# Performance work log

Measured on AMD Instinct MI355X. Metric: run time of the kernel, lower is better.

## Reference

```python
import jax, jax.numpy as jnp
import numpy as np

F_, V, ED = 16, 1000, 16
B = 65536
D_IN = F_ * ED            # 256
STAR = [256, 512, 256]    # star layers
FCN = [256, 128, 64]      # mmoe expert layers
DOM, TSK, EXP = 3, 2, 8
KDT = DOM * TSK           # 6 gates/towers
SKIP_WEIGHT = 0.5
EPS = 1e-5


def layernorm(x, g, b):
    mu = jnp.mean(x, -1, keepdims=True)
    var = jnp.mean((x - mu) ** 2, -1, keepdims=True)
    return (x - mu) * jax.lax.rsqrt(var + EPS) * g + b


def mlp1(x, W, b, g, be):
    # Linear -> LayerNorm -> ReLU (MLP_N with one block)
    return jax.nn.relu(layernorm(x @ W + b, g, be))


def stack2(h, W1, b1, g1, be1, W2, b2, g2, be2):
    # vectorized bank of 2-block MLP_N experts; h: [B,D0], W1: [E,D0,D1]
    h1 = jax.nn.relu(layernorm(jnp.einsum('bd,edh->ebh', h, W1) + b1[:, None, :], g1[:, None, :], be1[:, None, :]))
    h2 = jax.nn.relu(layernorm(jnp.einsum('ebd,edh->ebh', h1, W2) + b2[:, None, :], g2[:, None, :], be2[:, None, :]))
    return h2  # [E,B,H]


def setup_inputs() -> dict:
    key = jax.random.key(0)
    ks = iter(jax.random.split(key, 64))

    def nrm(shape, scale=0.05):
        return jax.random.normal(next(ks), shape, jnp.float32) * scale

    inp = {}
    inp['x'] = jax.random.randint(next(ks), (F_, B), 0, 3).astype(jnp.int32)
    inp['emb_tables'] = nrm((F_, V, ED))
    inp['skip_W'] = nrm((D_IN, STAR[2])); inp['skip_b'] = jnp.zeros((STAR[2],))
    inp['skip_g'] = jnp.ones((STAR[2],)); inp['skip_be'] = jnp.zeros((STAR[2],))
    inp['shared_W'] = nrm((STAR[0], STAR[1])); inp['shared_b'] = jnp.zeros((STAR[1],))
    inp['slot_W'] = nrm((DOM, STAR[0], STAR[1])); inp['slot_b'] = jnp.zeros((DOM, STAR[1]))
    inp['star_W'] = nrm((STAR[1], STAR[2])); inp['star_b'] = jnp.zeros((STAR[2],))
    inp['star_g'] = jnp.ones((STAR[2],)); inp['star_be'] = jnp.zeros((STAR[2],))
    inp['dskip_W'] = nrm((KDT, STAR[2], FCN[-1])); inp['dskip_b'] = jnp.zeros((KDT, FCN[-1]))
    inp['dskip_g'] = jnp.ones((KDT, FCN[-1])); inp['dskip_be'] = jnp.zeros((KDT, FCN[-1]))
    for pre, n in (('exp', EXP), ('dexp', DOM), ('texp', TSK)):
        inp[pre + '_W1'] = nrm((n, FCN[0], FCN[1])); inp[pre + '_b1'] = jnp.zeros((n, FCN[1]))
        inp[pre + '_g1'] = jnp.ones((n, FCN[1])); inp[pre + '_be1'] = jnp.zeros((n, FCN[1]))
        inp[pre + '_W2'] = nrm((n, FCN[1], FCN[2])); inp[pre + '_b2'] = jnp.zeros((n, FCN[2]))
        inp[pre + '_g2'] = jnp.ones((n, FCN[2])); inp[pre + '_be2'] = jnp.zeros((n, FCN[2]))
    inp['gate_W'] = nrm((KDT, FCN[0], EXP)); inp['gate_b'] = jnp.zeros((KDT, EXP))
    inp['tow_W1'] = nrm((KDT, FCN[-1], FCN[-1])); inp['tow_b1'] = jnp.zeros((KDT, FCN[-1]))
    inp['tow_g'] = jnp.ones((KDT, FCN[-1])); inp['tow_be'] = jnp.zeros((KDT, FCN[-1]))
    inp['tow_W2'] = nrm((KDT, FCN[-1])); inp['tow_b2'] = jnp.zeros((KDT,))
    return inp


def _forward(x, emb_tables, skip_W, skip_b, skip_g, skip_be, shared_W, shared_b,
             slot_W, slot_b, star_W, star_b, star_g, star_be,
             dskip_W, dskip_b, dskip_g, dskip_be,
             exp_W1, exp_b1, exp_g1, exp_be1, exp_W2, exp_b2, exp_g2, exp_be2,
             dexp_W1, dexp_b1, dexp_g1, dexp_be1, dexp_W2, dexp_b2, dexp_g2, dexp_be2,
             texp_W1, texp_b1, texp_g1, texp_be1, texp_W2, texp_b2, texp_g2, texp_be2,
             gate_W, gate_b, tow_W1, tow_b1, tow_g, tow_be, tow_W2, tow_b2):
    domain_id = x[-1]                                          # [B] in {0,1,2}
    embs = jax.vmap(lambda t, i: t[i])(emb_tables, x)          # [F,B,ED]
    input_emb = jnp.moveaxis(embs, 0, 1).reshape(x.shape[1], D_IN)  # [B,256]

    skip = mlp1(input_emb, skip_W, skip_b, skip_g, skip_be)    # [B,256]

    # STAR: per-domain elementwise-product weights, domain masked select
    slot_out = jnp.einsum('bd,kdh->kbh', input_emb, slot_W * shared_W[None]) + slot_b[:, None, :] + shared_b  # [D,B,512]
    onehot = (domain_id[None, :] == jnp.arange(DOM)[:, None]).astype(slot_out.dtype)  # [D,B]
    emb0 = jnp.sum(onehot[:, :, None] * slot_out, axis=0)      # [B,512]
    emb = mlp1(emb0, star_W, star_b, star_g, star_be) + skip   # [B,256]

    # gates use emb.detach()
    gate = jax.nn.softmax(jnp.einsum('bd,kde->kbe', jax.lax.stop_gradient(emb), gate_W) + gate_b[:, None, :], axis=-1)  # [6,B,8]

    fea = stack2(emb, exp_W1, exp_b1, exp_g1, exp_be1, exp_W2, exp_b2, exp_g2, exp_be2)        # [8,B,64]
    dfea = stack2(emb, dexp_W1, dexp_b1, dexp_g1, dexp_be1, dexp_W2, dexp_b2, dexp_g2, dexp_be2)  # [3,B,64]
    tfea = stack2(emb, texp_W1, texp_b1, texp_g1, texp_be1, texp_W2, texp_b2, texp_g2, texp_be2)  # [2,B,64]
    dskip = jax.nn.relu(layernorm(jnp.einsum('bd,kdh->kbh', emb, dskip_W) + dskip_b[:, None, :], dskip_g[:, None, :], dskip_be[:, None, :]))  # [6,B,64]

    d_idx = jnp.arange(KDT) % DOM
    t_idx = jnp.arange(KDT) % TSK
    fused = jnp.einsum('kbe,ebh->kbh', gate, fea) + dfea[d_idx] + tfea[t_idx] + SKIP_WEIGHT * dskip  # [6,B,64]

    h = jax.nn.relu(layernorm(jnp.einsum('kbh,khj->kbj', fused, tow_W1) + tow_b1[:, None, :], tow_g[:, None, :], tow_be[:, None, :]))
    probs = jax.nn.sigmoid(jnp.einsum('kbh,kh->kb', h, tow_W2) + tow_b2[:, None])  # [6,B]

    # output[:, i] with i = t*DOM + d -> [B,T,D]; pick per-sample domain column
    out = jnp.moveaxis(probs, 0, 1).reshape(-1, TSK, DOM)
    result = jnp.take_along_axis(out, domain_id[:, None, None].astype(jnp.int32), axis=2)[:, :, 0]  # [B,T]
    return result


def reference(x, emb_tables, skip_W, skip_b, skip_g, skip_be, shared_W, shared_b,
              slot_W, slot_b, star_W, star_b, star_g, star_be,
              dskip_W, dskip_b, dskip_g, dskip_be,
              exp_W1, exp_b1, exp_g1, exp_be1, exp_W2, exp_b2, exp_g2, exp_be2,
              dexp_W1, dexp_b1, dexp_g1, dexp_be1, dexp_W2, dexp_b2, dexp_g2, dexp_be2,
              texp_W1, texp_b1, texp_g1, texp_be1, texp_W2, texp_b2, texp_g2, texp_be2,
              gate_W, gate_b, tow_W1, tow_b1, tow_g, tow_be, tow_W2, tow_b2):
    return _forward(x, emb_tables, skip_W, skip_b, skip_g, skip_be, shared_W, shared_b,
                    slot_W, slot_b, star_W, star_b, star_g, star_be,
                    dskip_W, dskip_b, dskip_g, dskip_be,
                    exp_W1, exp_b1, exp_g1, exp_be1, exp_W2, exp_b2, exp_g2, exp_be2,
                    dexp_W1, dexp_b1, dexp_g1, dexp_be1, dexp_W2, dexp_b2, dexp_g2, dexp_be2,
                    texp_W1, texp_b1, texp_g1, texp_be1, texp_W2, texp_b2, texp_g2, texp_be2,
                    gate_W, gate_b, tow_W1, tow_b1, tow_g, tow_be, tow_W2, tow_b2)
```

## Files before the change

kernel.cpp:

```cpp
#include <hip/hip_runtime.h>
#include <stdint.h>

#define B_TOT 65536

typedef __attribute__((ext_vector_type(8))) short s16x8;
typedef __attribute__((ext_vector_type(4))) float f32x4;
typedef unsigned short u16;
typedef unsigned int u32;
typedef unsigned long long u64;

#define OFF_SKIPW   0
#define OFF_MD      65536
#define OFF_GATEW   262144
#define OFF_EXPW1   274432
#define OFF_EXPW2   700416
#define OFF_DSKIPW  806912
#define OFF_TOWW1   905216
#define OFF_BVEC    929792
#define OFF_PAR     931328
#define OFF_PARF    941568
#define OFF_EMB     944640
#define OFF_PERM    17852928
#define OFF_CNT     17985024

#define PAR_DSK  7488
#define PAR_TOW  8640
#define PAR_GB   10176
#define PAR_TB2  10224

__device__ __forceinline__ float bf2f(u16 h){ u32 v=((u32)h)<<16; return __builtin_bit_cast(float,v); }
__device__ __forceinline__ u16 f2bf(float f){
  u32 u=__builtin_bit_cast(u32,f);
  u += 0x7fffu + ((u>>16)&1u);
  return (u16)(u>>16);
}
__device__ __forceinline__ f32x4 mfma16(s16x8 a, s16x8 b, f32x4 c){
  return __builtin_amdgcn_mfma_f32_16x16x32_bf16(a,b,c,0,0,0);
}
__device__ __forceinline__ void lds_fence(){ asm volatile("s_waitcnt lgkmcnt(0)" ::: "memory"); }

__device__ __forceinline__ void gstage(const u16* gsrc, u16* ldsdst, int nbytes, int wv, int lane, int nw){
  for(int off = wv*1024; off < nbytes; off += nw*1024){
    __builtin_amdgcn_global_load_lds(
      (const __attribute__((address_space(1))) u32*)((const char*)gsrc + off + lane*16),
      (__attribute__((address_space(3))) u32*)((char*)ldsdst + off),
      16, 0, 0);
  }
}

template<int NT>
__device__ __forceinline__ void ln16(const f32x4* a, float invN, float* mu, float* rs){
  float s[4], q[4];
#pragma unroll
  for(int r=0;r<4;r++){ float aa=0.f,bb=0.f;
#pragma unroll
    for(int t=0;t<NT;t++){ float v=a[t][r]; aa+=v; bb+=v*v; }
    s[r]=aa; q[r]=bb; }
#pragma unroll
  for(int m=1;m<16;m<<=1){
#pragma unroll
    for(int r=0;r<4;r++){ s[r]+=__shfl_xor(s[r],m,16); q[r]+=__shfl_xor(q[r],m,16); } }
#pragma unroll
  for(int r=0;r<4;r++){ float m_=s[r]*invN; float v=q[r]*invN-m_*m_; mu[r]=m_; rs[r]=rsqrtf(v+1e-5f); }
}

__global__ __launch_bounds__(64) void k_sortinit(u16* __restrict__ ws){
  if(threadIdx.x<8) ((u32*)(ws+OFF_CNT))[threadIdx.x]=0u;
}
__global__ __launch_bounds__(256) void k_count(const int* __restrict__ x, u16* __restrict__ ws){
  u32* cnt=(u32*)(ws+OFF_CNT);
  int i=blockIdx.x*256+threadIdx.x;
  int lane=threadIdx.x&63;
  int d=x[15*B_TOT+i];
  u64 m0=__ballot(d==0), m1=__ballot(d==1), m2=__ballot(d==2);
  if(lane==0){
    if(m0) atomicAdd(&cnt[0],(u32)__popcll(m0));
    if(m1) atomicAdd(&cnt[1],(u32)__popcll(m1));
    if(m2) atomicAdd(&cnt[2],(u32)__popcll(m2));
  }
}
__global__ __launch_bounds__(256) void k_scatter(const int* __restrict__ x, u16* __restrict__ ws){
  u32* cnt=(u32*)(ws+OFF_CNT);
  u32* perm=(u32*)(ws+OFF_PERM);
  int i=blockIdx.x*256+threadIdx.x;
  int lane=threadIdx.x&63;
  int d=x[15*B_TOT+i];
  u32 c0=cnt[0], c1=cnt[1];
  u32 s1=c0, s2=c0+c1;
  u64 m0=__ballot(d==0), m1=__ballot(d==1), m2=__ballot(d==2);
  u32 b0v=0,b1v=0,b2v=0;
  if(lane==0){
    if(m0) b0v=atomicAdd(&cnt[3],(u32)__popcll(m0));
    if(m1) b1v=atomicAdd(&cnt[4],(u32)__popcll(m1));
    if(m2) b2v=atomicAdd(&cnt[5],(u32)__popcll(m2));
  }
  b0v=__shfl(b0v,0,64); b1v=__shfl(b1v,0,64); b2v=__shfl(b2v,0,64);
  u64 below=(1ull<<lane)-1ull;
  u32 pos;
  if(d==0)      pos=    b0v+(u32)__popcll(m0&below);
  else if(d==1) pos=s1+ b1v+(u32)__popcll(m1&below);
  else          pos=s2+ b2v+(u32)__popcll(m2&below);
  perm[pos]=(u32)i;
}

__global__ __launch_bounds__(256) void k_pack(
    const float* __restrict__ skip_W, const float* __restrict__ gate_W,
    const float* __restrict__ exp_W1, const float* __restrict__ dexp_W1, const float* __restrict__ texp_W1,
    const float* __restrict__ exp_W2, const float* __restrict__ dexp_W2, const float* __restrict__ texp_W2,
    const float* __restrict__ dskip_W, const float* __restrict__ tow_W1,
    u16* __restrict__ ws)
{
  int i=blockIdx.x*256+threadIdx.x;
  if(i>=OFF_BVEC) return;
  if(i>=OFF_MD && i<OFF_GATEW) return;
  float v;
  if(i<OFF_MD){
    int l=i; int j=l&7, lane=(l>>3)&63, kt=(l>>9)&7, ct=l>>12;
    int n=ct*16+(lane&15), k=kt*32+((lane>>4)<<3)+j;
    v = skip_W[k*256+n];
  } else if(i<OFF_EXPW1){
    int l=i-OFF_GATEW; int j=l&7, lane=(l>>3)&63, kt=(l>>9)&7, ct=l>>12;
    int n=ct*16+(lane&15), k=kt*32+((lane>>4)<<3)+j;
    int k6=n>>3, e=n&7;
    v = gate_W[(k6*256+k)*8+e];
  } else if(i<OFF_EXPW2){
    int l=i-OFF_EXPW1; int e=l>>15, r=l&32767;
    int j=r&7, lane=(r>>3)&63, kt=(r>>9)&7, ct=r>>12;
    int n=ct*16+(lane&15), k=kt*32+((lane>>4)<<3)+j;
    v = (e<8)? exp_W1[(e*256+k)*128+n] : (e<11)? dexp_W1[((e-8)*256+k)*128+n] : texp_W1[((e-11)*256+k)*128+n];
  } else if(i<OFF_DSKIPW){
    int l=i-OFF_EXPW2; int e=l>>13, r=l&8191;
    int j=r&7, lane=(r>>3)&63, kt=(r>>9)&3, ct=r>>11;
    int n=ct*16+(lane&15), k=kt*32+((lane>>4)<<3)+j;
    v = (e<8)? exp_W2[(e*128+k)*64+n] : (e<11)? dexp_W2[((e-8)*128+k)*64+n] : texp_W2[((e-11)*128+k)*64+n];
  } else if(i<OFF_TOWW1){
    int l=i-OFF_DSKIPW; int s=l>>14, r=l&16383;
    int j=r&7, lane=(r>>3)&63, kt=(r>>9)&7, ct=r>>12;
    int n=ct*16+(lane&15), k=kt*32+((lane>>4)<<3)+j;
    v = dskip_W[(s*256+k)*64+n];
  } else {
    int l=i-OFF_TOWW1; int s=l>>12, r=l&4095;
    int j=r&7, lane=(r>>3)&63, kt=(r>>9)&1, ct=r>>10;
    int n=ct*16+(lane&15), k=kt*32+((lane>>4)<<3)+j;
    v = tow_W1[(s*64+k)*64+n];
  }
  ws[i]=f2bf(v);
}

__global__ __launch_bounds__(256) void k_packpar(
    const float* __restrict__ exp_b1,const float* __restrict__ exp_g1,const float* __restrict__ exp_be1,
    const float* __restrict__ exp_b2,const float* __restrict__ exp_g2,const float* __restrict__ exp_be2,
    const float* __restrict__ dexp_b1,const float* __restrict__ dexp_g1,const float* __restrict__ dexp_be1,
    const float* __restrict__ dexp_b2,const float* __restrict__ dexp_g2,const float* __restrict__ dexp_be2,
    const float* __restrict__ texp_b1,const float* __restrict__ texp_g1,const float* __restrict__ texp_be1,
    const float* __restrict__ texp_b2,const float* __restrict__ texp_g2,const float* __restrict__ texp_be2,
    const float* __restrict__ dskip_b,const float* __restrict__ dskip_g,const float* __restrict__ dskip_be,
    const float* __restrict__ gate_b,
    const float* __restrict__ tow_b1,const float* __restrict__ tow_g,const float* __restrict__ tow_be,
    const float* __restrict__ tow_W2,const float* __restrict__ tow_b2,
    const float* __restrict__ skip_b,const float* __restrict__ skip_g,const float* __restrict__ skip_be,
    const float* __restrict__ star_b,const float* __restrict__ star_g,const float* __restrict__ star_be,
    u16* __restrict__ ws)
{
  int i=blockIdx.x*256+threadIdx.x;
  float* parf=(float*)(ws+OFF_PARF);
  if(i<10240){
    float v=0.f;
    if(i<PAR_DSK){
      int e=i/576, r=i%576;
      const float *b1,*g1,*be1,*b2,*g2,*be2;
      if(e<8){ b1=exp_b1+e*128; g1=exp_g1+e*128; be1=exp_be1+e*128;
               b2=exp_b2+e*64;  g2=exp_g2+e*64;  be2=exp_be2+e*64; }
      else if(e<11){ int q=e-8; b1=dexp_b1+q*128; g1=dexp_g1+q*128; be1=dexp_be1+q*128;
               b2=dexp_b2+q*64; g2=dexp_g2+q*64; be2=dexp_be2+q*64; }
      else { int q=e-11; b1=texp_b1+q*128; g1=texp_g1+q*128; be1=texp_be1+q*128;
               b2=texp_b2+q*64; g2=texp_g2+q*64; be2=texp_be2+q*64; }
      v = (r<128)? b1[r] : (r<256)? g1[r-128] : (r<384)? be1[r-256]
        : (r<448)? b2[r-384] : (r<512)? g2[r-448] : be2[r-512];
    } else if(i<PAR_TOW){
      int l=i-PAR_DSK; int j=l/192, r=l%192;
      v = (r<64)? dskip_b[j*64+r] : (r<128)? dskip_g[j*64+r-64] : dskip_be[j*64+r-128];
    } else if(i<PAR_GB){
      int l=i-PAR_TOW; int k6=l/256, r=l%256;
      v = (r<64)? tow_b1[k6*64+r] : (r<128)? tow_g[k6*64+r-64]
        : (r<192)? tow_be[k6*64+r-128] : tow_W2[k6*64+r-192];
    } else if(i<PAR_TB2){ v=gate_b[i-PAR_GB]; }
    else if(i<PAR_TB2+6){ v=tow_b2[i-PAR_TB2]; }
    ws[OFF_PAR+i]=f2bf(v);
  } else if(i<10240+1536){
    int l=i-10240;
    parf[l] = (l<256)? skip_b[l] : (l<512)? skip_g[l-256] : (l<768)? skip_be[l-512]
            : (l<1024)? star_b[l-768] : (l<1280)? star_g[l-1024] : star_be[l-1280];
  }
}

__global__ __launch_bounds__(256) void k_fold(
    const float* __restrict__ slot_W, const float* __restrict__ shared_W, const float* __restrict__ star_W,
    const float* __restrict__ slot_b, const float* __restrict__ shared_b,
    u16* __restrict__ ws)
{
  __shared__ float w[512];
  int bid=blockIdx.x, tid=threadIdx.x;
  if(bid<768){
    int d=bid>>8, k=bid&255;
    for(int j=tid;j<512;j+=256) w[j]=slot_W[(d*256+k)*512+j]*shared_W[k*512+j];
    __syncthreads();
    int n=tid; float a=0.f;
    for(int j=0;j<512;j++) a += w[j]*star_W[j*256+n];
    int ct=n>>4, l15=n&15, kt=k>>5, hi=(k>>3)&3, j8=k&7;
    ws[OFF_MD + d*65536 + (((ct*8+kt)*64 + hi*16 + l15)<<3) + j8] = f2bf(a);
  } else {
    int d=bid-768;
    for(int j=tid;j<512;j+=256) w[j]=slot_b[d*512+j]+shared_b[j];
    __syncthreads();
    int n=tid; float a=0.f;
    for(int j=0;j<512;j++) a += w[j]*star_W[j*256+n];
    ((float*)(ws+OFF_BVEC))[d*256+n]=a;
  }
}

__global__ __launch_bounds__(256,2) void k_front(
    const int* __restrict__ x, const float* __restrict__ emb_tables,
    u16* __restrict__ wsu)
{
  __shared__ __align__(16) u16 shbuf[33792];
  __shared__ float bvecL[768];
  __shared__ float parF[1536];

  const int tid=threadIdx.x, lane=tid&63, wv=tid>>6;
  const int l15=lane&15, hq=lane>>4;
  const int b0=blockIdx.x*128, rowbase=b0+wv*32;
  const f32x4 fz={0.f,0.f,0.f,0.f};
  const s16x8 zf={0,0,0,0,0,0,0,0};
  u16* Wb[2]={shbuf, shbuf+8192};
  u16* trbw = shbuf + wv*8448;
  u16* embp = wsu+OFF_EMB;
  const u32* perm=(const u32*)(wsu+OFF_PERM);

  gstage(wsu+OFF_SKIPW, Wb[0], 16384, wv, lane, 4);
  gstage(wsu+OFF_BVEC, (u16*)bvecL, 3072, wv, lane, 4);
  gstage(wsu+OFF_PARF, (u16*)parF, 6144, wv, lane, 4);

  const int dlo=__builtin_amdgcn_readfirstlane(x[15*B_TOT+(int)perm[b0]]);
  const int dhi=__builtin_amdgcn_readfirstlane(x[15*B_TOT+(int)perm[b0+127]]);

  int dmA[2], dm[2][4];
  s16x8 af[2][8];
#pragma unroll
  for(int rt=0;rt<2;rt++){
    int prow=(int)perm[rowbase+rt*16+l15];
    dmA[rt]=x[15*B_TOT+prow];
#pragma unroll
    for(int r=0;r<4;r++) dm[rt][r]=x[15*B_TOT+(int)perm[rowbase+rt*16+hq*4+r]];
#pragma unroll
    for(int kt=0;kt<8;kt++){
      int f=kt*2+(hq>>1), j0=(hq&1)*8;
      int idx=x[f*B_TOT+prow];
      const float* sp=emb_tables + (size_t)(f*1000+idx)*16 + j0;
      float4 v0=*(const float4*)sp, v1=*(const float4*)(sp+4);
      union{ u16 h[8]; s16x8 v; } t;
      t.h[0]=f2bf(v0.x); t.h[1]=f2bf(v0.y); t.h[2]=f2bf(v0.z); t.h[3]=f2bf(v0.w);
      t.h[4]=f2bf(v1.x); t.h[5]=f2bf(v1.y); t.h[6]=f2bf(v1.z); t.h[7]=f2bf(v1.w);
      af[rt][kt]=t.v;
    }
  }
  __syncthreads();
  int cur=0;

  f32x4 acc[2][16];
#pragma unroll
  for(int rt=0;rt<2;rt++)
#pragma unroll
    for(int ct=0;ct<16;ct++) acc[rt][ct]=fz;

#pragma unroll
  for(int c=0;c<8;c++){
    if(c<7) gstage(wsu+OFF_SKIPW+(c+1)*8192, Wb[cur^1], 16384, wv, lane, 4);
    const u16* B=Wb[cur];
#pragma unroll
    for(int kt=0;kt<8;kt++){
#pragma unroll
      for(int i=0;i<2;i++){
        s16x8 bf=*(const s16x8*)(B + (((i*8+kt)*64+lane)<<3));
        acc[0][c*2+i]=mfma16(af[0][kt],bf,acc[0][c*2+i]);
        acc[1][c*2+i]=mfma16(af[1][kt],bf,acc[1][c*2+i]);
      }
    }
    __syncthreads(); cur^=1;
  }
#pragma unroll
  for(int rt=0;rt<2;rt++){
#pragma unroll
    for(int ct=0;ct<16;ct++){ float bb=parF[ct*16+l15];
#pragma unroll
      for(int r=0;r<4;r++) acc[rt][ct][r]+=bb; }
    float mu[4],rs[4];
    ln16<16>(&acc[rt][0], 1.f/256.f, mu, rs);
#pragma unroll
    for(int ct=0;ct<16;ct++){
      int col=ct*16+l15;
      float gv=parF[256+col], bev=parF[512+col];
#pragma unroll
      for(int r=0;r<4;r++){
        float v=fmaxf((acc[rt][ct][r]-mu[r])*rs[r]*gv+bev,0.f);
        trbw[(rt*16+hq*4+r)*264 + col]=f2bf(v);
      }
    }
  }
  lds_fence();
#pragma unroll
  for(int rt=0;rt<2;rt++){
    int rtg=(b0>>4)+wv*2+rt;
#pragma unroll
    for(int kt=0;kt<8;kt++){
      s16x8 v=*(const s16x8*)(trbw + (rt*16+l15)*264 + kt*32+hq*8);
      *(s16x8*)(embp + (((size_t)(rtg*8+kt)*64+lane)<<3)) = v;
    }
  }
  __syncthreads();
  gstage(wsu+OFF_MD+dlo*65536, Wb[0], 16384, wv, lane, 4);
  __syncthreads();
  cur=0;

#pragma unroll
  for(int rt=0;rt<2;rt++)
#pragma unroll
    for(int ct=0;ct<16;ct++) acc[rt][ct]=fz;
  for(int dd=dlo;dd<=dhi;dd++){
#pragma unroll
    for(int c=0;c<8;c++){
      if(c<7)        gstage(wsu+OFF_MD+dd*65536+(c+1)*8192, Wb[cur^1], 16384, wv, lane, 4);
      else if(dd<dhi) gstage(wsu+OFF_MD+(dd+1)*65536,       Wb[cur^1], 16384, wv, lane, 4);
      const u16* B=Wb[cur];
#pragma unroll
      for(int kt=0;kt<8;kt++){
        s16x8 a0=(dmA[0]==dd)?af[0][kt]:zf;
        s16x8 a1=(dmA[1]==dd)?af[1][kt]:zf;
#pragma unroll
        for(int i=0;i<2;i++){
          s16x8 bf=*(const s16x8*)(B + (((i*8+kt)*64+lane)<<3));
          acc[0][c*2+i]=mfma16(a0,bf,acc[0][c*2+i]);
          acc[1][c*2+i]=mfma16(a1,bf,acc[1][c*2+i]);
        }
      }
      __syncthreads(); cur^=1;
    }
  }

#pragma unroll
  for(int rt=0;rt<2;rt++){
#pragma unroll
    for(int ct=0;ct<16;ct++){
      int col=ct*16+l15; float sb=parF[768+col];
#pragma unroll
      for(int r=0;r<4;r++) acc[rt][ct][r] += sb + bvecL[dm[rt][r]*256+col];
    }
    float mu[4],rs[4];
    ln16<16>(&acc[rt][0], 1.f/256.f, mu, rs);
#pragma unroll
    for(int ct=0;ct<16;ct++){
      int col=ct*16+l15;
      float gv=parF[1024+col], bev=parF[1280+col];
#pragma unroll
      for(int r=0;r<4;r++){
        float v=fmaxf((acc[rt][ct][r]-mu[r])*rs[r]*gv+bev,0.f);
        trbw[(rt*16+hq*4+r)*264 + col]=f2bf(v);
      }
    }
  }
  lds_fence();
#pragma unroll
  for(int rt=0;rt<2;rt++){
    int rtg=(b0>>4)+wv*2+rt;
#pragma unroll
    for(int kt=0;kt<8;kt++){
      s16x8 vs=*(const s16x8*)(trbw + (rt*16+l15)*264 + kt*32+hq*8);
      s16x8 vk=*(const s16x8*)(embp + (((size_t)(rtg*8+kt)*64+lane)<<3));
      union{ u16 h[8]; s16x8 v; } t;
#pragma unroll
      for(int j=0;j<8;j++) t.h[j]=f2bf(bf2f((u16)vs[j])+bf2f((u16)vk[j]));
      *(s16x8*)(embp + (((size_t)(rtg*8+kt)*64+lane)<<3)) = t.v;
    }
  }
}

__device__ __forceinline__ void stage8k(const u16* g, u16* l, int wv, int lane){
  __builtin_amdgcn_global_load_lds(
    (const __attribute__((address_space(1))) u32*)((const char*)g + wv*1024 + lane*16),
    (__attribute__((address_space(3))) u32*)((char*)l + wv*1024), 16,0,0);
}
__device__ __forceinline__ void stage16k(const u16* g, u16* l, int wv, int lane){
  stage8k(g,      l,      wv, lane);
  stage8k(g+4096, l+4096, wv, lane);
}
__device__ __forceinline__ void stage_phase_u(int p, int dlo, int ndom,
    const u16* wsu, u16* slot, int wv, int lane){
  const int NU=10+ndom;
  const int P1=2+5*NU, P2=P1+4*ndom;
  if(p<2){ stage16k(wsu+OFF_GATEW+p*8192, slot, wv, lane); return; }
  if(p<P1){ int q=p-2, ui=q/5, s=q%5;
    int u = (ui<8)? ui : (ui<8+ndom)? (8+dlo+(ui-8)) : (11+(ui-8-ndom));
    const u16* g = (s<4)? (wsu+OFF_EXPW1+u*32768+s*8192) : (wsu+OFF_EXPW2+u*8192);
    stage16k(g, slot, wv, lane); return; }
  if(p<P2){ int q=p-P1; int dd=dlo+(q>>2); int j=(q&2)?(3+dd):dd; int half=q&1;
    stage16k(wsu+OFF_DSKIPW+j*16384+half*8192, slot, wv, lane); return; }
  { int dd=dlo+(p-P2);
    stage8k(wsu+OFF_TOWW1+dd*4096,     slot,      wv, lane);
    stage8k(wsu+OFF_TOWW1+(3+dd)*4096, slot+4096, wv, lane); }
}
__device__ __forceinline__ void endph2(){ asm volatile("s_waitcnt vmcnt(2)\n\ts_barrier" ::: "memory"); }
__device__ __forceinline__ void endph0(){ asm volatile("s_waitcnt vmcnt(0)\n\ts_barrier" ::: "memory"); }
#define ENDPH(pp) do{ if((pp)+2<P3) endph2(); else if((pp)+2==P3) endph0(); }while(0)

__global__ __launch_bounds__(512,2) void k_B(
    const int* __restrict__ x, u16* __restrict__ wsu, float* __restrict__ out)
{
  __shared__ __align__(16) u16 Wb[3][8192];
  __shared__ __align__(16) u16 trb[8][32][136];
  __shared__ __align__(16) u16 parAll[10240];
  __shared__ __align__(16) u32 gateF[256][8];

  const int tid=threadIdx.x, lane=tid&63, wv=tid>>6;
  const int l15=lane&15, hq=lane>>4;
  const int b0=blockIdx.x*256, rowbase=b0+wv*32;
  const f32x4 fz={0.f,0.f,0.f,0.f};
  const u16* embp=wsu+OFF_EMB;
  const u32* perm=(const u32*)(wsu+OFF_PERM);
  u16* trbw=&trb[wv][0][0];

  gstage(wsu+OFF_PAR, parAll, 20480, wv, lane, 8);

  const int dlo=__builtin_amdgcn_readfirstlane(x[15*B_TOT+(int)perm[b0]]);
  const int dhi=__builtin_amdgcn_readfirstlane(x[15*B_TOT+(int)perm[b0+255]]);
  const int ndom=dhi-dlo+1;
  const int NU=10+ndom;
  const int P1=2+5*NU, P2=P1+4*ndom, P3=P2+ndom;

  stage16k(wsu+OFF_GATEW,      &Wb[0][0], wv, lane);
  stage16k(wsu+OFF_GATEW+8192, &Wb[1][0], wv, lane);

  u32 pv[2][4]; int dm[2][4];
#pragma unroll
  for(int rt=0;rt<2;rt++)
#pragma unroll
    for(int r=0;r<4;r++){
      u32 pp=perm[rowbase + rt*16 + hq*4 + r];
      pv[rt][r]=pp;
      dm[rt][r]=x[15*B_TOT+(int)pp];
    }

  s16x8 af[2][8];
#pragma unroll
  for(int rt=0;rt<2;rt++){
    int rtg=(rowbase>>4)+rt;
#pragma unroll
    for(int kt=0;kt<8;kt++)
      af[rt][kt]=*(const s16x8*)(embp + (((size_t)(rtg*8+kt)*64+lane)<<3));
  }

  f32x4 fa0[2][4], fa1[2][4];
#pragma unroll
  for(int rt=0;rt<2;rt++)
#pragma unroll
    for(int ct=0;ct<4;ct++){ fa0[rt][ct]=fz; fa1[rt][ct]=fz; }

  __syncthreads();
  int p=0;

  {
    f32x4 gacc[2][3];
#pragma unroll
    for(int rt=0;rt<2;rt++)
#pragma unroll
      for(int ct=0;ct<3;ct++) gacc[rt][ct]=fz;
    stage_phase_u(2, dlo, ndom, wsu, &Wb[2][0], wv, lane);
#pragma unroll
    for(int kt=0;kt<8;kt++)
#pragma unroll
      for(int i=0;i<2;i++){
        s16x8 bf=*(const s16x8*)(&Wb[0][0] + (((i*8+kt)*64+lane)<<3));
        gacc[0][i]=mfma16(af[0][kt],bf,gacc[0][i]);
        gacc[1][i]=mfma16(af[1][kt],bf,gacc[1][i]);
      }
    ENDPH(0); p=1;

    stage_phase_u(3, dlo, ndom, wsu, &Wb[0][0], wv, lane);
#pragma unroll
    for(int kt=0;kt<8;kt++){
      s16x8 bf=*(const s16x8*)(&Wb[1][0] + ((kt*64+lane)<<3));
      gacc[0][2]=mfma16(af[0][kt],bf,gacc[0][2]);
      gacc[1][2]=mfma16(af[1][kt],bf,gacc[1][2]);
    }
    u16* gFh=(u16*)&gateF[0][0];
#pragma unroll
    for(int rt=0;rt<2;rt++)
#pragma unroll
      for(int ct=0;ct<3;ct++){
        int k6=ct*2+(l15>>3), e=l15&7;
        float gb=bf2f(parAll[PAR_GB + k6*8+e]);
#pragma unroll
        for(int r=0;r<4;r++){
          float v=gacc[rt][ct][r]+gb;
          float mx=v;
          mx=fmaxf(mx,__shfl_xor(mx,1,8)); mx=fmaxf(mx,__shfl_xor(mx,2,8)); mx=fmaxf(mx,__shfl_xor(mx,4,8));
          float pe=__expf(v-mx);
          float ss=pe;
          ss+=__shfl_xor(ss,1,8); ss+=__shfl_xor(ss,2,8); ss+=__shfl_xor(ss,4,8);
          int brow=wv*32+rt*16+hq*4+r;
          int dmv=dm[rt][r];
          if(k6==dmv)   gFh[(brow*8+e)*2]  =f2bf(pe/ss);
          if(k6==3+dmv) gFh[(brow*8+e)*2+1]=f2bf(pe/ss);
        }
      }
    lds_fence();
    ENDPH(1); p=2;
  }

  for(int ui=0;ui<NU;ui++){
    const int u = (ui<8)? ui : (ui<8+ndom)? (8+dlo+(ui-8)) : (11+(ui-8-ndom));
    f32x4 acc1[2][8];
#pragma unroll
    for(int rt=0;rt<2;rt++)
#pragma unroll
      for(int ct=0;ct<8;ct++) acc1[rt][ct]=fz;
    for(int c=0;c<4;c++){
      const u16* Bw=&Wb[p%3][0];
      if(p+2<P3) stage_phase_u(p+2, dlo, ndom, wsu, &Wb[(p+2)%3][0], wv, lane);
#pragma unroll
      for(int kt=0;kt<8;kt++)
#pragma unroll
        for(int i=0;i<2;i++){
          s16x8 bf=*(const s16x8*)(Bw + (((i*8+kt)*64+lane)<<3));
          acc1[0][c*2+i]=mfma16(af[0][kt],bf,acc1[0][c*2+i]);
          acc1[1][c*2+i]=mfma16(af[1][kt],bf,acc1[1][c*2+i]);
        }
      ENDPH(p); p++;
    }
    {
      const u16* Bw=&Wb[p%3][0];
      if(p+2<P3) stage_phase_u(p+2, dlo, ndom, wsu, &Wb[(p+2)%3][0], wv, lane);
      const int pb=u*576;
#pragma unroll
      for(int rt=0;rt<2;rt++){
#pragma unroll
        for(int ct=0;ct<8;ct++){ float bb=bf2f(parAll[pb+ct*16+l15]);
#pragma unroll
          for(int r=0;r<4;r++) acc1[rt][ct][r]+=bb; }
        float mu[4],rs[4],nm[4];
        ln16<8>(&acc1[rt][0],1.f/128.f,mu,rs);
#pragma unroll
        for(int r=0;r<4;r++) nm[r]=-mu[r]*rs[r];
#pragma unroll
        for(int ct=0;ct<8;ct++){
          int col=ct*16+l15;
          float gv=bf2f(parAll[pb+128+col]), bev=bf2f(parAll[pb+256+col]);
#pragma unroll
          for(int r=0;r<4;r++){
            float vn=fmaf(acc1[rt][ct][r],rs[r],nm[r]);
            trbw[(rt*16+hq*4+r)*136+col]=f2bf(fmaxf(fmaf(vn,gv,bev),0.f));
          }
        }
      }
      lds_fence();
      s16x8 af2[2][4];
#pragma unroll
      for(int rt=0;rt<2;rt++)
#pragma unroll
        for(int kt=0;kt<4;kt++)
          af2[rt][kt]=*(const s16x8*)(trbw+(rt*16+l15)*136+kt*32+hq*8);
      f32x4 acc2[2][4];
#pragma unroll
      for(int rt=0;rt<2;rt++)
#pragma unroll
        for(int ct=0;ct<4;ct++) acc2[rt][ct]=fz;
#pragma unroll
      for(int kt=0;kt<4;kt++)
#pragma unroll
        for(int ct=0;ct<4;ct++){
          s16x8 bf=*(const s16x8*)(Bw + (((ct*4+kt)*64+lane)<<3));
          acc2[0][ct]=mfma16(af2[0][kt],bf,acc2[0][ct]);
          acc2[1][ct]=mfma16(af2[1][kt],bf,acc2[1][ct]);
        }
#pragma unroll
      for(int rt=0;rt<2;rt++){
#pragma unroll
        for(int ct=0;ct<4;ct++){ float bb=bf2f(parAll[pb+384+ct*16+l15]);
#pragma unroll
          for(int r=0;r<4;r++) acc2[rt][ct][r]+=bb; }
        float mu[4],rs[4],nm[4];
        ln16<4>(&acc2[rt][0],1.f/64.f,mu,rs);
#pragma unroll
        for(int r=0;r<4;r++) nm[r]=-mu[r]*rs[r];
        float g0v[4],g1v[4];
        if(ui<8){
#pragma unroll
          for(int r=0;r<4;r++){ u32 gg=gateF[wv*32+rt*16+hq*4+r][ui];
            g0v[r]=bf2f((u16)(gg&0xffffu)); g1v[r]=bf2f((u16)(gg>>16)); }
        } else if(ui<8+ndom){
          int du=dlo+(ui-8);
#pragma unroll
          for(int r=0;r<4;r++){ float m=(dm[rt][r]==du)?1.f:0.f; g0v[r]=m; g1v[r]=m; }
        } else {
          int q=ui-8-ndom;
#pragma unroll
          for(int r=0;r<4;r++){
            g0v[r]=((dm[rt][r]&1)==q)?1.f:0.f;
            g1v[r]=(((dm[rt][r]+1)&1)==q)?1.f:0.f;
          }
        }
#pragma unroll
        for(int ct=0;ct<4;ct++){
          int col=ct*16+l15;
          float gv=bf2f(parAll[pb+448+col]), bev=bf2f(parAll[pb+512+col]);
#pragma unroll
          for(int r=0;r<4;r++){
            float vn=fmaf(acc2[rt][ct][r],rs[r],nm[r]);
            float o=fmaxf(fmaf(vn,gv,bev),0.f);
            fa0[rt][ct][r]=fmaf(g0v[r],o,fa0[rt][ct][r]);
            fa1[rt][ct][r]=fmaf(g1v[r],o,fa1[rt][ct][r]);
          }
        }
      }
      ENDPH(p); p++;
    }
  }

  for(int dq=0;dq<2*ndom;dq++){
    const int dd=dlo+(dq>>1);
    const int jj=(dq&1)? (3+dd) : dd;
    f32x4 a3[2][4];
#pragma unroll
    for(int rt=0;rt<2;rt++)
#pragma unroll
      for(int ct=0;ct<4;ct++) a3[rt][ct]=fz;
    for(int c=0;c<2;c++){
      const u16* Bw=&Wb[p%3][0];
      if(p+2<P3) stage_phase_u(p+2, dlo, ndom, wsu, &Wb[(p+2)%3][0], wv, lane);
#pragma unroll
      for(int kt=0;kt<8;kt++)
#pragma unroll
        for(int i=0;i<2;i++){
          s16x8 bf=*(const s16x8*)(Bw + (((i*8+kt)*64+lane)<<3));
          a3[0][c*2+i]=mfma16(af[0][kt],bf,a3[0][c*2+i]);
          a3[1][c*2+i]=mfma16(af[1][kt],bf,a3[1][c*2+i]);
        }
      if(c==1){
        const int pb=PAR_DSK+jj*192;
#pragma unroll
        for(int rt=0;rt<2;rt++){
#pragma unroll
          for(int ct=0;ct<4;ct++){ float bb=bf2f(parAll[pb+ct*16+l15]);
#pragma unroll
            for(int r=0;r<4;r++) a3[rt][ct][r]+=bb; }
          float mu[4],rs[4],nm[4],mk[4];
          ln16<4>(&a3[rt][0],1.f/64.f,mu,rs);
#pragma unroll
          for(int r=0;r<4;r++){ nm[r]=-mu[r]*rs[r]; mk[r]=(dm[rt][r]==dd)?0.5f:0.f; }
#pragma unroll
          for(int ct=0;ct<4;ct++){
            int col=ct*16+l15;
            float gv=bf2f(parAll[pb+64+col]), bev=bf2f(parAll[pb+128+col]);
#pragma unroll
            for(int r=0;r<4;r++){
              float vn=fmaf(a3[rt][ct][r],rs[r],nm[r]);
              float o=fmaxf(fmaf(vn,gv,bev),0.f);
              if((dq&1)==0) fa0[rt][ct][r]=fmaf(mk[r],o,fa0[rt][ct][r]);
              else          fa1[rt][ct][r]=fmaf(mk[r],o,fa1[rt][ct][r]);
            }
          }
        }
      }
      ENDPH(p); p++;
    }
  }

#pragma unroll
  for(int rt=0;rt<2;rt++)
#pragma unroll
    for(int ct=0;ct<4;ct++)
#pragma unroll
      for(int r=0;r<4;r++){
        int rr=(rt*16+hq*4+r)*136 + ct*16+l15;
        trbw[rr]   =f2bf(fa0[rt][ct][r]);
        trbw[rr+64]=f2bf(fa1[rt][ct][r]);
      }
  lds_fence();
  s16x8 aft0[2][2], aft1[2][2];
#pragma unroll
  for(int rt=0;rt<2;rt++)
#pragma unroll
    for(int kt=0;kt<2;kt++){
      aft0[rt][kt]=*(const s16x8*)(trbw+(rt*16+l15)*136+kt*32+hq*8);
      aft1[rt][kt]=*(const s16x8*)(trbw+(rt*16+l15)*136+64+kt*32+hq*8);
    }

  for(int t=0;t<ndom;t++){
    const u16* Bw=&Wb[p%3][0];
    if(p+2<P3) stage_phase_u(p+2, dlo, ndom, wsu, &Wb[(p+2)%3][0], wv, lane);
    const int dd=dlo+t;
#pragma unroll
    for(int s=0;s<2;s++){
      const int k6 = s? (3+dd) : dd;
      f32x4 ta[2][4];
#pragma unroll
      for(int rt=0;rt<2;rt++)
#pragma unroll
        for(int ct=0;ct<4;ct++) ta[rt][ct]=fz;
#pragma unroll
      for(int kt=0;kt<2;kt++)
#pragma unroll
        for(int ct=0;ct<4;ct++){
          s16x8 bf=*(const s16x8*)(Bw + s*4096 + (((ct*2+kt)*64+lane)<<3));
          if(s==0){ ta[0][ct]=mfma16(aft0[0][kt],bf,ta[0][ct]); ta[1][ct]=mfma16(aft0[1][kt],bf,ta[1][ct]); }
          else    { ta[0][ct]=mfma16(aft1[0][kt],bf,ta[0][ct]); ta[1][ct]=mfma16(aft1[1][kt],bf,ta[1][ct]); }
        }
      const int pb=PAR_TOW+k6*256;
#pragma unroll
      for(int rt=0;rt<2;rt++){
#pragma unroll
        for(int ct=0;ct<4;ct++){ float bb=bf2f(parAll[pb+ct*16+l15]);
#pragma unroll
          for(int r=0;r<4;r++) ta[rt][ct][r]+=bb; }
        float mu[4],rs[4],nm[4];
        ln16<4>(&ta[rt][0],1.f/64.f,mu,rs);
#pragma unroll
        for(int r=0;r<4;r++) nm[r]=-mu[r]*rs[r];
        float pr[4]={0.f,0.f,0.f,0.f};
#pragma unroll
        for(int ct=0;ct<4;ct++){
          int col=ct*16+l15;
          float gv=bf2f(parAll[pb+64+col]), bev=bf2f(parAll[pb+128+col]), w2=bf2f(parAll[pb+192+col]);
#pragma unroll
          for(int r=0;r<4;r++){
            float vn=fmaf(ta[rt][ct][r],rs[r],nm[r]);
            float o=fmaxf(fmaf(vn,gv,bev),0.f);
            pr[r]=fmaf(o,w2,pr[r]);
          }
        }
#pragma unroll
        for(int m=1;m<16;m<<=1){
#pragma unroll
          for(int r=0;r<4;r++) pr[r]+=__shfl_xor(pr[r],m,16);
        }
        if(l15==0){
          float tb2=bf2f(parAll[PAR_TB2+k6]);
#pragma unroll
          for(int r=0;r<4;r++){
            if(dm[rt][r]==dd){
              float sv=pr[r]+tb2;
              out[(size_t)pv[rt][r]*2 + s] = 1.f/(1.f+__expf(-sv));
            }
          }
        }
      }
    }
    ENDPH(p); p++;
  }
}

extern "C" void kernel_launch(void* const* d_in, const int* in_sizes, int n_in,
                              void* d_out, int out_size, void* d_ws, size_t ws_size,
                              hipStream_t stream)
{
  if(ws_size < (size_t)(OFF_CNT+32)*2) return;

  const int*   x          =(const int*)  d_in[0];
  const float* emb_tables =(const float*)d_in[1];
  const float* skip_W     =(const float*)d_in[2];
  const float* skip_b     =(const float*)d_in[3];
  const float* skip_g     =(const float*)d_in[4];
  const float* skip_be    =(const float*)d_in[5];
  const float* shared_W   =(const float*)d_in[6];
  const float* shared_b   =(const float*)d_in[7];
  const float* slot_W     =(const float*)d_in[8];
  const float* slot_b     =(const float*)d_in[9];
  const float* star_W     =(const float*)d_in[10];
  const float* star_b     =(const float*)d_in[11];
  const float* star_g     =(const float*)d_in[12];
  const float* star_be    =(const float*)d_in[13];
  const float* dskip_W    =(const float*)d_in[14];
  const float* dskip_b    =(const float*)d_in[15];
  const float* dskip_g    =(const float*)d_in[16];
  const float* dskip_be   =(const float*)d_in[17];
  const float* exp_W1     =(const float*)d_in[18];
  const float* exp_b1     =(const float*)d_in[19];
  const float* exp_g1     =(const float*)d_in[20];
  const float* exp_be1    =(const float*)d_in[21];
  const float* exp_W2     =(const float*)d_in[22];
  const float* exp_b2     =(const float*)d_in[23];
  const float* exp_g2     =(const float*)d_in[24];
  const float* exp_be2    =(const float*)d_in[25];
  const float* dexp_W1    =(const float*)d_in[26];
  const float* dexp_b1    =(const float*)d_in[27];
  const float* dexp_g1    =(const float*)d_in[28];
  const float* dexp_be1   =(const float*)d_in[29];
  const float* dexp_W2    =(const float*)d_in[30];
  const float* dexp_b2    =(const float*)d_in[31];
  const float* dexp_g2    =(const float*)d_in[32];
  const float* dexp_be2   =(const float*)d_in[33];
  const float* texp_W1    =(const float*)d_in[34];
  const float* texp_b1    =(const float*)d_in[35];
  const float* texp_g1    =(const float*)d_in[36];
  const float* texp_be1   =(const float*)d_in[37];
  const float* texp_W2    =(const float*)d_in[38];
  const float* texp_b2    =(const float*)d_in[39];
  const float* texp_g2    =(const float*)d_in[40];
  const float* texp_be2   =(const float*)d_in[41];
  const float* gate_W     =(const float*)d_in[42];
  const float* gate_b     =(const float*)d_in[43];
  const float* tow_W1     =(const float*)d_in[44];
  const float* tow_b1     =(const float*)d_in[45];
  const float* tow_g      =(const float*)d_in[46];
  const float* tow_be     =(const float*)d_in[47];
  const float* tow_W2     =(const float*)d_in[48];
  const float* tow_b2     =(const float*)d_in[49];

  u16* wsu=(u16*)d_ws;
  float* out=(float*)d_out;

  k_sortinit<<<1,64,0,stream>>>(wsu);
  k_count<<<B_TOT/256,256,0,stream>>>(x,wsu);
  k_scatter<<<B_TOT/256,256,0,stream>>>(x,wsu);
  k_pack<<<(OFF_BVEC+255)/256,256,0,stream>>>(skip_W,gate_W,
      exp_W1,dexp_W1,texp_W1,exp_W2,dexp_W2,texp_W2,dskip_W,tow_W1,wsu);
  k_packpar<<<46,256,0,stream>>>(
      exp_b1,exp_g1,exp_be1,exp_b2,exp_g2,exp_be2,
      dexp_b1,dexp_g1,dexp_be1,dexp_b2,dexp_g2,dexp_be2,
      texp_b1,texp_g1,texp_be1,texp_b2,texp_g2,texp_be2,
      dskip_b,dskip_g,dskip_be,gate_b,
      tow_b1,tow_g,tow_be,tow_W2,tow_b2,
      skip_b,skip_g,skip_be,star_b,star_g,star_be,wsu);
  k_fold<<<771,256,0,stream>>>(slot_W,shared_W,star_W,slot_b,shared_b,wsu);
  k_front<<<B_TOT/128,256,0,stream>>>(x,emb_tables,wsu);
  k_B<<<B_TOT/256,512,0,stream>>>(x,wsu,out);
}
```

Baseline: 409.2 us.

## Halve k_B block size, double-buffer weights, read expert params from global

```diff
diff --git a/kernel.cpp b/kernel.cpp
--- a/kernel.cpp
+++ b/kernel.cpp
@@ -37,7 +37,10 @@
 __device__ __forceinline__ f32x4 mfma16(s16x8 a, s16x8 b, f32x4 c){
   return __builtin_amdgcn_mfma_f32_16x16x32_bf16(a,b,c,0,0,0);
 }
-__device__ __forceinline__ void lds_fence(){ asm volatile("s_waitcnt lgkmcnt(0)" ::: "memory"); }
+__device__ __forceinline__ void lds_fence(){
+  asm volatile("s_waitcnt lgkmcnt(0)" ::: "memory");
+  __builtin_amdgcn_sched_barrier(0);
+}
 
 __device__ __forceinline__ void gstage(const u16* gsrc, u16* ldsdst, int nbytes, int wv, int lane, int nw){
   for(int off = wv*1024; off < nbytes; off += nw*1024){
@@ -384,60 +387,64 @@
   }
 }
 
-__device__ __forceinline__ void stage8k(const u16* g, u16* l, int wv, int lane){
+__device__ __forceinline__ void glds1k(const u16* g, u16* l, int lane){
   __builtin_amdgcn_global_load_lds(
-    (const __attribute__((address_space(1))) u32*)((const char*)g + wv*1024 + lane*16),
-    (__attribute__((address_space(3))) u32*)((char*)l + wv*1024), 16,0,0);
-}
-__device__ __forceinline__ void stage16k(const u16* g, u16* l, int wv, int lane){
-  stage8k(g,      l,      wv, lane);
-  stage8k(g+4096, l+4096, wv, lane);
-}
-__device__ __forceinline__ void stage_phase_u(int p, int dlo, int ndom,
+    (const __attribute__((address_space(1))) u32*)((const char*)g + lane*16),
+    (__attribute__((address_space(3))) u32*)((char*)l), 16,0,0);
+}
+__device__ __forceinline__ void stage16k4(const u16* g, u16* l, int wv, int lane){
+#pragma unroll
+  for(int q=0;q<4;q++) glds1k(g + wv*2048 + q*512, l + wv*2048 + q*512, lane);
+}
+__device__ __forceinline__ void stage8k4(const u16* g, u16* l, int wv, int lane){
+#pragma unroll
+  for(int q=0;q<2;q++) glds1k(g + wv*1024 + q*512, l + wv*1024 + q*512, lane);
+}
+__device__ __forceinline__ void stage_phase4(int p, int dlo, int ndom,
     const u16* wsu, u16* slot, int wv, int lane){
   const int NU=10+ndom;
   const int P1=2+5*NU, P2=P1+4*ndom;
-  if(p<2){ stage16k(wsu+OFF_GATEW+p*8192, slot, wv, lane); return; }
+  if(p<2){ stage16k4(wsu+OFF_GATEW+p*8192, slot, wv, lane); return; }
   if(p<P1){ int q=p-2, ui=q/5, s=q%5;
     int u = (ui<8)? ui : (ui<8+ndom)? (8+dlo+(ui-8)) : (11+(ui-8-ndom));
     const u16* g = (s<4)? (wsu+OFF_EXPW1+u*32768+s*8192) : (wsu+OFF_EXPW2+u*8192);
-    stage16k(g, slot, wv, lane); return; }
+    stage16k4(g, slot, wv, lane); return; }
   if(p<P2){ int q=p-P1; int dd=dlo+(q>>2); int j=(q&2)?(3+dd):dd; int half=q&1;
-    stage16k(wsu+OFF_DSKIPW+j*16384+half*8192, slot, wv, lane); return; }
+    stage16k4(wsu+OFF_DSKIPW+j*16384+half*8192, slot, wv, lane); return; }
   { int dd=dlo+(p-P2);
-    stage8k(wsu+OFF_TOWW1+dd*4096,     slot,      wv, lane);
-    stage8k(wsu+OFF_TOWW1+(3+dd)*4096, slot+4096, wv, lane); }
-}
-__device__ __forceinline__ void endph2(){ asm volatile("s_waitcnt vmcnt(2)\n\ts_barrier" ::: "memory"); }
-__device__ __forceinline__ void endph0(){ asm volatile("s_waitcnt vmcnt(0)\n\ts_barrier" ::: "memory"); }
-#define ENDPH(pp) do{ if((pp)+2<P3) endph2(); else if((pp)+2==P3) endph0(); }while(0)
-
-__global__ __launch_bounds__(512,2) void k_B(
+    stage8k4(wsu+OFF_TOWW1+dd*4096,     slot,      wv, lane);
+    stage8k4(wsu+OFF_TOWW1+(3+dd)*4096, slot+4096, wv, lane); }
+}
+__device__ __forceinline__ void endph(){
+  asm volatile("s_waitcnt vmcnt(0) lgkmcnt(0)\n\ts_barrier" ::: "memory");
+  __builtin_amdgcn_sched_barrier(0);
+}
+
+__global__ __launch_bounds__(256,2) void k_B(
     const int* __restrict__ x, u16* __restrict__ wsu, float* __restrict__ out)
 {
-  __shared__ __align__(16) u16 Wb[3][8192];
-  __shared__ __align__(16) u16 trb[8][32][136];
-  __shared__ __align__(16) u16 parAll[10240];
-  __shared__ __align__(16) u32 gateF[256][8];
+  __shared__ __align__(16) u16 Wb[2][8192];
+  __shared__ __align__(16) u16 trb[4][32][136];
+  __shared__ __align__(16) u32 gateF[128][8];
+  __shared__ __align__(16) u16 parT[4096];
 
   const int tid=threadIdx.x, lane=tid&63, wv=tid>>6;
   const int l15=lane&15, hq=lane>>4;
-  const int b0=blockIdx.x*256, rowbase=b0+wv*32;
+  const int b0=blockIdx.x*128, rowbase=b0+wv*32;
   const f32x4 fz={0.f,0.f,0.f,0.f};
   const u16* embp=wsu+OFF_EMB;
+  const u16* parE=wsu+OFF_PAR;
   const u32* perm=(const u32*)(wsu+OFF_PERM);
   u16* trbw=&trb[wv][0][0];
 
-  gstage(wsu+OFF_PAR, parAll, 20480, wv, lane, 8);
-
   const int dlo=__builtin_amdgcn_readfirstlane(x[15*B_TOT+(int)perm[b0]]);
-  const int dhi=__builtin_amdgcn_readfirstlane(x[15*B_TOT+(int)perm[b0+255]]);
+  const int dhi=__builtin_amdgcn_readfirstlane(x[15*B_TOT+(int)perm[b0+127]]);
   const int ndom=dhi-dlo+1;
   const int NU=10+ndom;
   const int P1=2+5*NU, P2=P1+4*ndom, P3=P2+ndom;
 
-  stage16k(wsu+OFF_GATEW,      &Wb[0][0], wv, lane);
-  stage16k(wsu+OFF_GATEW+8192, &Wb[1][0], wv, lane);
+  stage_phase4(0, dlo, ndom, wsu, &Wb[0][0], wv, lane);
+  stage8k4(wsu+OFF_PAR+PAR_DSK, parT, wv, lane);
 
   u32 pv[2][4]; int dm[2][4];
 #pragma unroll
@@ -464,6 +471,7 @@
 #pragma unroll
     for(int ct=0;ct<4;ct++){ fa0[rt][ct]=fz; fa1[rt][ct]=fz; }
 
+  asm volatile("s_waitcnt vmcnt(0)" ::: "memory");
   __syncthreads();
   int p=0;
 
@@ -473,7 +481,7 @@
     for(int rt=0;rt<2;rt++)
 #pragma unroll
       for(int ct=0;ct<3;ct++) gacc[rt][ct]=fz;
-    stage_phase_u(2, dlo, ndom, wsu, &Wb[2][0], wv, lane);
+    stage_phase4(1, dlo, ndom, wsu, &Wb[1][0], wv, lane);
 #pragma unroll
     for(int kt=0;kt<8;kt++)
 #pragma unroll
@@ -482,9 +490,9 @@
         gacc[0][i]=mfma16(af[0][kt],bf,gacc[0][i]);
         gacc[1][i]=mfma16(af[1][kt],bf,gacc[1][i]);
       }
-    ENDPH(0); p=1;
-
-    stage_phase_u(3, dlo, ndom, wsu, &Wb[0][0], wv, lane);
+    endph(); p=1;
+
+    stage_phase4(2, dlo, ndom, wsu, &Wb[0][0], wv, lane);
 #pragma unroll
     for(int kt=0;kt<8;kt++){
       s16x8 bf=*(const s16x8*)(&Wb[1][0] + ((kt*64+lane)<<3));
@@ -497,7 +505,7 @@
 #pragma unroll
       for(int ct=0;ct<3;ct++){
         int k6=ct*2+(l15>>3), e=l15&7;
-        float gb=bf2f(parAll[PAR_GB + k6*8+e]);
+        float gb=bf2f(parT[(PAR_GB-PAR_DSK) + k6*8+e]);
 #pragma unroll
         for(int r=0;r<4;r++){
           float v=gacc[rt][ct][r]+gb;
@@ -513,7 +521,7 @@
         }
       }
     lds_fence();
-    ENDPH(1); p=2;
+    endph(); p=2;
   }
 
   for(int ui=0;ui<NU;ui++){
@@ -524,8 +532,8 @@
 #pragma unroll
       for(int ct=0;ct<8;ct++) acc1[rt][ct]=fz;
     for(int c=0;c<4;c++){
-      const u16* Bw=&Wb[p%3][0];
-      if(p+2<P3) stage_phase_u(p+2, dlo, ndom, wsu, &Wb[(p+2)%3][0], wv, lane);
+      const u16* Bw=&Wb[p&1][0];
+      if(p+1<P3) stage_phase4(p+1, dlo, ndom, wsu, &Wb[(p+1)&1][0], wv, lane);
 #pragma unroll
       for(int kt=0;kt<8;kt++)
 #pragma unroll
@@ -534,16 +542,16 @@
           acc1[0][c*2+i]=mfma16(af[0][kt],bf,acc1[0][c*2+i]);
           acc1[1][c*2+i]=mfma16(af[1][kt],bf,acc1[1][c*2+i]);
         }
-      ENDPH(p); p++;
+      endph(); p++;
     }
     {
-      const u16* Bw=&Wb[p%3][0];
-      if(p+2<P3) stage_phase_u(p+2, dlo, ndom, wsu, &Wb[(p+2)%3][0], wv, lane);
-      const int pb=u*576;
+      const u16* Bw=&Wb[p&1][0];
+      if(p+1<P3) stage_phase4(p+1, dlo, ndom, wsu, &Wb[(p+1)&1][0], wv, lane);
+      const u16* pe_=parE + u*576;
 #pragma unroll
       for(int rt=0;rt<2;rt++){
 #pragma unroll
-        for(int ct=0;ct<8;ct++){ float bb=bf2f(parAll[pb+ct*16+l15]);
+        for(int ct=0;ct<8;ct++){ float bb=bf2f(pe_[ct*16+l15]);
 #pragma unroll
           for(int r=0;r<4;r++) acc1[rt][ct][r]+=bb; }
         float mu[4],rs[4],nm[4];
@@ -553,7 +561,7 @@
 #pragma unroll
         for(int ct=0;ct<8;ct++){
           int col=ct*16+l15;
-          float gv=bf2f(parAll[pb+128+col]), bev=bf2f(parAll[pb+256+col]);
+          float gv=bf2f(pe_[128+col]), bev=bf2f(pe_[256+col]);
 #pragma unroll
           for(int r=0;r<4;r++){
             float vn=fmaf(acc1[rt][ct][r],rs[r],nm[r]);
@@ -584,7 +592,7 @@
 #pragma unroll
       for(int rt=0;rt<2;rt++){
 #pragma unroll
-        for(int ct=0;ct<4;ct++){ float bb=bf2f(parAll[pb+384+ct*16+l15]);
+        for(int ct=0;ct<4;ct++){ float bb=bf2f(pe_[384+ct*16+l15]);
 #pragma unroll
           for(int r=0;r<4;r++) acc2[rt][ct][r]+=bb; }
         float mu[4],rs[4],nm[4];
@@ -611,7 +619,7 @@
 #pragma unroll
         for(int ct=0;ct<4;ct++){
           int col=ct*16+l15;
-          float gv=bf2f(parAll[pb+448+col]), bev=bf2f(parAll[pb+512+col]);
+          float gv=bf2f(pe_[448+col]), bev=bf2f(pe_[512+col]);
 #pragma unroll
           for(int r=0;r<4;r++){
             float vn=fmaf(acc2[rt][ct][r],rs[r],nm[r]);
@@ -621,7 +629,7 @@
           }
         }
       }
-      ENDPH(p); p++;
+      endph(); p++;
     }
   }
 
@@ -634,8 +642,8 @@
 #pragma unroll
       for(int ct=0;ct<4;ct++) a3[rt][ct]=fz;
     for(int c=0;c<2;c++){
-      const u16* Bw=&Wb[p%3][0];
-      if(p+2<P3) stage_phase_u(p+2, dlo, ndom, wsu, &Wb[(p+2)%3][0], wv, lane);
+      const u16* Bw=&Wb[p&1][0];
+      if(p+1<P3) stage_phase4(p+1, dlo, ndom, wsu, &Wb[(p+1)&1][0], wv, lane);
 #pragma unroll
       for(int kt=0;kt<8;kt++)
 #pragma unroll
@@ -645,11 +653,11 @@
           a3[1][c*2+i]=mfma16(af[1][kt],bf,a3[1][c*2+i]);
         }
       if(c==1){
-        const int pb=PAR_DSK+jj*192;
+        const int pb=jj*192;
 #pragma unroll
         for(int rt=0;rt<2;rt++){
 #pragma unroll
-          for(int ct=0;ct<4;ct++){ float bb=bf2f(parAll[pb+ct*16+l15]);
+          for(int ct=0;ct<4;ct++){ float bb=bf2f(parT[pb+ct*16+l15]);
 #pragma unroll
             for(int r=0;r<4;r++) a3[rt][ct][r]+=bb; }
           float mu[4],rs[4],nm[4],mk[4];
@@ -659,7 +667,7 @@
 #pragma unroll
           for(int ct=0;ct<4;ct++){
             int col=ct*16+l15;
-            float gv=bf2f(parAll[pb+64+col]), bev=bf2f(parAll[pb+128+col]);
+            float gv=bf2f(parT[pb+64+col]), bev=bf2f(parT[pb+128+col]);
 #pragma unroll
             for(int r=0;r<4;r++){
               float vn=fmaf(a3[rt][ct][r],rs[r],nm[r]);
@@ -670,7 +678,7 @@
           }
         }
       }
-      ENDPH(p); p++;
+      endph(); p++;
     }
   }
 
@@ -695,8 +703,8 @@
     }
 
   for(int t=0;t<ndom;t++){
-    const u16* Bw=&Wb[p%3][0];
-    if(p+2<P3) stage_phase_u(p+2, dlo, ndom, wsu, &Wb[(p+2)%3][0], wv, lane);
+    const u16* Bw=&Wb[p&1][0];
+    if(p+1<P3) stage_phase4(p+1, dlo, ndom, wsu, &Wb[(p+1)&1][0], wv, lane);
     const int dd=dlo+t;
 #pragma unroll
     for(int s=0;s<2;s++){
@@ -714,11 +722,11 @@
           if(s==0){ ta[0][ct]=mfma16(aft0[0][kt],bf,ta[0][ct]); ta[1][ct]=mfma16(aft0[1][kt],bf,ta[1][ct]); }
           else    { ta[0][ct]=mfma16(aft1[0][kt],bf,ta[0][ct]); ta[1][ct]=mfma16(aft1[1][kt],bf,ta[1][ct]); }
         }
-      const int pb=PAR_TOW+k6*256;
+      const int pb=(PAR_TOW-PAR_DSK)+k6*256;
 #pragma unroll
       for(int rt=0;rt<2;rt++){
 #pragma unroll
-        for(int ct=0;ct<4;ct++){ float bb=bf2f(parAll[pb+ct*16+l15]);
+        for(int ct=0;ct<4;ct++){ float bb=bf2f(parT[pb+ct*16+l15]);
 #pragma unroll
           for(int r=0;r<4;r++) ta[rt][ct][r]+=bb; }
         float mu[4],rs[4],nm[4];
@@ -729,7 +737,7 @@
 #pragma unroll
         for(int ct=0;ct<4;ct++){
           int col=ct*16+l15;
-          float gv=bf2f(parAll[pb+64+col]), bev=bf2f(parAll[pb+128+col]), w2=bf2f(parAll[pb+192+col]);
+          float gv=bf2f(parT[pb+64+col]), bev=bf2f(parT[pb+128+col]), w2=bf2f(parT[pb+192+col]);
 #pragma unroll
           for(int r=0;r<4;r++){
             float vn=fmaf(ta[rt][ct][r],rs[r],nm[r]);
@@ -743,7 +751,7 @@
           for(int r=0;r<4;r++) pr[r]+=__shfl_xor(pr[r],m,16);
         }
         if(l15==0){
-          float tb2=bf2f(parAll[PAR_TB2+k6]);
+          float tb2=bf2f(parT[(PAR_TB2-PAR_DSK)+k6]);
 #pragma unroll
           for(int r=0;r<4;r++){
             if(dm[rt][r]==dd){
@@ -754,7 +762,8 @@
         }
       }
     }
-    ENDPH(p); p++;
+    if(p+1<P3) endph();
+    p++;
   }
 }
 
@@ -832,5 +841,5 @@
       skip_b,skip_g,skip_be,star_b,star_g,star_be,wsu);
   k_fold<<<771,256,0,stream>>>(slot_W,shared_W,star_W,slot_b,shared_b,wsu);
   k_front<<<B_TOT/128,256,0,stream>>>(x,emb_tables,wsu);
-  k_B<<<B_TOT/256,512,0,stream>>>(x,wsu,out);
-}
+  k_B<<<B_TOT/128,256,0,stream>>>(x,wsu,out);
+}
```

Measured after the change: 402.9 us. About the same (-1.5%).
